# Kernel tuning notes

Measured on AMD Instinct MI355X. Metric: run time of the kernel, lower is better.

Reference implementation:

```python
import jax, jax.numpy as jnp
import numpy as np
import math

HIDDEN = 256
INPUT_SIZE = 32

def setup_inputs() -> dict:
    key = jax.random.key(0)
    k1, k2, k3 = jax.random.split(key, 3)
    stdv = 1.0 / math.sqrt(HIDDEN)
    inp = jax.random.normal(k1, (32, 48, 24, INPUT_SIZE), dtype=jnp.float32)
    W = jax.random.uniform(k2, (6 * HIDDEN, INPUT_SIZE + 2 * HIDDEN), minval=-stdv, maxval=stdv, dtype=jnp.float32)
    Bp = jax.random.uniform(k3, (6 * HIDDEN,), minval=-stdv, maxval=stdv, dtype=jnp.float32)
    return {"input": inp, "W": W, "Bp": Bp}

def _witran_forward(input, W, Bp):
    B, rows, cols, C = input.shape
    H = W.shape[0] // 6
    # flag == 1: permute to (cols, batch, rows, C)
    x = jnp.transpose(input, (2, 0, 1, 3))
    R = cols            # Water2sea_slice_num
    Lorig = rows        # Original_slice_len
    L = R + Lorig - 1   # Water2sea_slice_len
    # input_transfer: row r occupies slice positions r : r+Lorig (pad then roll)
    padded = jnp.pad(x, ((0, 0), (0, 0), (0, R - 1), (0, 0)))        # (R, B, L, C)
    shifted = jax.vmap(lambda xr, r: jnp.roll(xr, r, axis=1))(padded, jnp.arange(R))
    a = shifted.reshape(R * B, L, C)
    a_slices = jnp.transpose(a, (1, 0, 2))                            # (L, R*B, C)
    r_idx = jnp.repeat(jnp.arange(R), B)                              # (R*B,)

    def step(carry, inp):
        h_row, h_col = carry
        s, xs = inp
        # bias applied only to first (s+1)*B rows and only while s < R (faithful to torch)
        mask = ((r_idx <= s) & (s < R)).astype(xs.dtype)[:, None]
        gate = jnp.concatenate([h_row, h_col, xs], axis=-1) @ W.T + mask * Bp
        sig = jax.nn.sigmoid(gate[:, : 4 * H])
        tg = jnp.tanh(gate[:, 4 * H:])
        u_row, o_row, u_col, o_col = jnp.split(sig, 4, axis=-1)
        i_row, i_col = jnp.split(tg, 2, axis=-1)
        h_row = jnp.tanh((1.0 - u_row) * h_row + u_row * i_row) * o_row
        h_col_new = jnp.tanh((1.0 - u_col) * h_col + u_col * i_col) * o_col
        # roll col hidden down by one batch block for next diagonal
        h_col_rolled = jnp.roll(h_col_new, B, axis=0)
        return (h_row, h_col_rolled), (h_row, h_col_new)

    init = (jnp.zeros((R * B, H), input.dtype), jnp.zeros((R * B, H), input.dtype))
    _, (rows_all, cols_all) = jax.lax.scan(step, init, (jnp.arange(L), a_slices))
    # output_all_slice: stack along slice dim -> (R*B, L, 2H)
    output_all = jnp.transpose(jnp.concatenate([rows_all, cols_all], axis=-1), (1, 0, 2))
    rows_r = rows_all.reshape(L, R, B, H)
    cols_r = cols_all.reshape(L, R, B, H)
    # row hidden saved at slice s = Lorig-1+k from block k (diagonal)
    hidden_row = rows_r[jnp.arange(Lorig - 1, L), jnp.arange(R)]      # (R, B, H)
    # col hidden saved at slices s >= R-1 from the last block (pre-roll)
    hidden_col = cols_r[R - 1:, R - 1]                                # (Lorig, B, H)
    hidden_row_all = jnp.transpose(hidden_row, (1, 0, 2)).reshape(B, 1, R, H)
    hidden_col_all = jnp.transpose(hidden_col, (1, 0, 2)).reshape(B, 1, Lorig, H)
    # flag == 1 return order: (output, hidden_col_all, hidden_row_all)
    return output_all, hidden_col_all, hidden_row_all

def reference(input, W, Bp):
    return _witran_forward(input, W, Bp)
```

## Files before the change

kernel.cpp:

```cpp
#include <hip/hip_runtime.h>
#include <cstddef>


namespace {
constexpr int H_   = 256;
constexpr int R_   = 24;
constexpr int LOR_ = 48;
constexpr int L_   = 71;
constexpr int N_   = 768;
constexpr int KH_  = 512;
constexpr int KT_  = 544;
constexpr int AST_ = 552;
}

typedef __attribute__((ext_vector_type(8))) _Float16       f16x8;
typedef __attribute__((ext_vector_type(8))) unsigned short u16x8;
typedef __attribute__((ext_vector_type(4))) float          f32x4;
typedef __attribute__((ext_vector_type(2))) float          f32x2;

__device__ __forceinline__ float fsig(float x)  { return 1.f / (1.f + __expf(-x)); }
__device__ __forceinline__ float ftanhf(float x){ float e = __expf(2.f * x); return 1.f - 2.f / (e + 1.f); }

__global__ __launch_bounds__(256) void prep_all(const float* __restrict__ W,
                                                const float* __restrict__ inp,
                                                _Float16* __restrict__ Wfrag,
                                                _Float16* __restrict__ xall,
                                                unsigned long long* __restrict__ zb) {
    const int bx = blockIdx.x;
    const int t  = threadIdx.x;
    if (bx < 3264) {
        int o = bx * 256 + t;
        int j8   = o & 7;
        int lane = (o >> 3) & 63;
        int rest = o >> 9;
        int lt   = rest % 96;
        int kc   = rest / 96;
        int n0 = lane & 15, quad = lane >> 4;
        int lg  = lt * 16 + n0;
        int kt  = lg / 96;
        int rem = lg % 96;
        int g  = rem >> 4, kl = rem & 15;
        int j  = g * 256 + kt * 16 + kl;
        int kg = kc * 32 + quad * 8 + j8;
        Wfrag[o] = (_Float16)W[j * KT_ + kg];
    } else if (bx < 10080) {
        int o = (bx - 3264) * 256 + t;
        int c = o & 31;
        int n = (o >> 5) % N_;
        int s = (o >> 5) / N_;
        int r = n >> 5, b = n & 31;
        int l = s - r;
        float v = 0.f;
        if (l >= 0 && l < LOR_) v = inp[((b * LOR_ + l) * R_ + r) * 32 + c];
        xall[o] = (_Float16)v;
    } else {
        zb[(bx - 10080) * 256 + t] = 0ull;
    }
}

__global__ __launch_bounds__(384, 2) void step_k(
    const _Float16* __restrict__ Wfrag,
    const _Float16* __restrict__ xall,
    const _Float16* __restrict__ hbc,
    _Float16*       __restrict__ hbn,
    const float* __restrict__ Bp,
    float* __restrict__ out0, float* __restrict__ out1, float* __restrict__ out2,
    int s)
{
    __shared__ unsigned short As[48 * AST_];
    __shared__ float Gt[48][98];

    const int t    = threadIdx.x;
    const int wv   = t >> 6;
    const int lane = t & 63;
    const int n0   = lane & 15;
    const int quad = lane >> 4;
    const int kt   = blockIdx.x & 15;
    const int mc   = blockIdx.x >> 4;

    f16x8 bfr[17];
#pragma unroll
    for (int kc = 0; kc < 17; ++kc)
        bfr[kc] = *(const f16x8*)(const void*)(
            Wfrag + ((size_t)(kc * 96 + kt * 6 + wv) * 64 + lane) * 8);

    f16x8 xf[3];
#pragma unroll
    for (int mt = 0; mt < 3; ++mt)
        xf[mt] = *(const f16x8*)(const void*)(
            xall + ((size_t)(s * N_ + mc * 48 + mt * 16 + n0)) * 32 + quad * 8);

    const int mm = t >> 3;
    const int kp = (t & 7) * 2;
    const int n  = mc * 48 + mm;
    const int k  = kt * 16 + kp;
    f32x2 bp[6];
    if (s < R_) {
#pragma unroll
        for (int g = 0; g < 6; ++g)
            bp[g] = *(const f32x2*)(const void*)(Bp + g * 256 + k);
    }

#pragma unroll
    for (int it = 0; it < 8; ++it) {
        int q   = it * 384 + t;
        int row = q >> 6;
        int col = (q & 63) * 8;
        *(u16x8*)(void*)(&As[row * AST_ + col]) =
            *(const u16x8*)(const void*)((const unsigned short*)hbc +
                                         (size_t)(mc * 48 + row) * KH_ + col);
    }
    __syncthreads();

    f32x4 acc[3];
#pragma unroll
    for (int mt = 0; mt < 3; ++mt) acc[mt] = (f32x4){0.f, 0.f, 0.f, 0.f};

#pragma unroll
    for (int kc = 0; kc < 16; ++kc) {
        f16x8 a[3];
#pragma unroll
        for (int mt = 0; mt < 3; ++mt)
            a[mt] = *(const f16x8*)(const void*)(
                &As[(mt * 16 + n0) * AST_ + kc * 32 + quad * 8]);
#pragma unroll
        for (int mt = 0; mt < 3; ++mt)
            acc[mt] = __builtin_amdgcn_mfma_f32_16x16x32_f16(a[mt], bfr[kc], acc[mt], 0, 0, 0);
    }
#pragma unroll
    for (int mt = 0; mt < 3; ++mt)
        acc[mt] = __builtin_amdgcn_mfma_f32_16x16x32_f16(xf[mt], bfr[16], acc[mt], 0, 0, 0);

#pragma unroll
    for (int mt = 0; mt < 3; ++mt)
#pragma unroll
        for (int reg = 0; reg < 4; ++reg)
            Gt[mt * 16 + quad * 4 + reg][wv * 16 + n0] = acc[mt][reg];

    __syncthreads();

    {
        const int r  = n >> 5, b = n & 31;
        const bool useb = (r <= s) && (s < R_);

        f32x2 gv[6];
#pragma unroll
        for (int g = 0; g < 6; ++g) {
            f32x2 v = *(const f32x2*)(const void*)&Gt[mm][g * 16 + kp];
            gv[g] = useb ? (v + bp[g]) : v;
        }

        const _Float16* hrow = (const _Float16*)(const void*)&As[mm * AST_ + k];
        const _Float16* hcol = (const _Float16*)(const void*)&As[mm * AST_ + 256 + k];
        f32x2 hro = { (float)hrow[0], (float)hrow[1] };
        f32x2 hco = { (float)hcol[0], (float)hcol[1] };

        f32x2 hrv, hcv;
#pragma unroll
        for (int j = 0; j < 2; ++j) {
            float ur = fsig(gv[0][j]);
            float oR = fsig(gv[1][j]);
            float uc = fsig(gv[2][j]);
            float oc = fsig(gv[3][j]);
            float ir = ftanhf(gv[4][j]);
            float ic = ftanhf(gv[5][j]);
            hrv[j] = ftanhf((1.f - ur) * hro[j] + ur * ir) * oR;
            hcv[j] = ftanhf((1.f - uc) * hco[j] + uc * ic) * oc;
        }

        float* o0 = out0 + ((size_t)n * L_ + s) * 512;
        __builtin_nontemporal_store(hrv, (f32x2*)(void*)(o0 + k));
        __builtin_nontemporal_store(hcv, (f32x2*)(void*)(o0 + 256 + k));

        int n2 = n + 32; if (n2 >= N_) n2 -= N_;

        union { _Float16 h[2]; unsigned int u; } pr, pc;
        pr.h[0] = (_Float16)hrv[0]; pr.h[1] = (_Float16)hrv[1];
        pc.h[0] = (_Float16)hcv[0]; pc.h[1] = (_Float16)hcv[1];
        *(unsigned int*)(void*)(hbn + (size_t)n  * KH_ + k)       = pr.u;
        *(unsigned int*)(void*)(hbn + (size_t)n2 * KH_ + 256 + k) = pc.u;

        if (s >= LOR_ - 1 && r == s - (LOR_ - 1))
            __builtin_nontemporal_store(hrv, (f32x2*)(void*)(out2 + (size_t)(b * R_ + r) * H_ + k));
        if (r == R_ - 1 && s >= R_ - 1)
            __builtin_nontemporal_store(hcv, (f32x2*)(void*)(out1 + (size_t)(b * LOR_ + (s - (R_ - 1))) * H_ + k));
    }
}

extern "C" void kernel_launch(void* const* d_in, const int* in_sizes, int n_in,
                              void* d_out, int out_size, void* d_ws, size_t ws_size,
                              hipStream_t stream) {
    const float* inp = (const float*)d_in[0];
    const float* W   = (const float*)d_in[1];
    const float* Bp  = (const float*)d_in[2];

    float* out0 = (float*)d_out;
    float* out1 = out0 + (size_t)N_ * L_ * 512;
    float* out2 = out1 + (size_t)32 * LOR_ * H_;

    char* ws = (char*)d_ws;
    _Float16* Wfrag = (_Float16*)(ws);
    _Float16* xall  = (_Float16*)(ws + 1671168);
    _Float16* hb0   = (_Float16*)(ws + 5160960);
    _Float16* hb1   = (_Float16*)(ws + 5947392);

    prep_all<<<10848, 256, 0, stream>>>(W, inp, Wfrag, xall,
                                        (unsigned long long*)hb0);

    for (int s = 0; s < L_; ++s) {
        const _Float16* hbc = (s & 1) ? hb1 : hb0;
        _Float16*       hbn = (s & 1) ? hb0 : hb1;
        int act = (s < 23 ? s : 23) + 1;
        int nmc = (32 * act + 47) / 48;
        step_k<<<nmc * 16, 384, 0, stream>>>(Wfrag, xall, hbc, hbn,
                                             Bp, out0, out1, out2, s);
    }
}
```

Before: 616.6 us.

## Split K reduction across two wave groups with 768-thread blocks

Doubles the block to 768 threads and splits the 17 MFMA K-chunks between two groups of six waves. Each group writes partial gate sums to its own shared-memory tile, and the epilogue adds the two tiles before the gate activations. Each thread now handles one output element instead of two. For steps from 22 onward, the block-index mapping is also permuted to interleave mc across blocks. The aim is to halve per-wave serial MFMA latency and register pressure in this latency-bound per-step kernel, at the cost of more shared memory, an extra reduction, and narrower stores.

```diff
diff --git a/kernel.cpp b/kernel.cpp
--- a/kernel.cpp
+++ b/kernel.cpp
@@ -16,7 +16,6 @@
 typedef __attribute__((ext_vector_type(8))) _Float16       f16x8;
 typedef __attribute__((ext_vector_type(8))) unsigned short u16x8;
 typedef __attribute__((ext_vector_type(4))) float          f32x4;
-typedef __attribute__((ext_vector_type(2))) float          f32x2;
 
 __device__ __forceinline__ float fsig(float x)  { return 1.f / (1.f + __expf(-x)); }
 __device__ __forceinline__ float ftanhf(float x){ float e = __expf(2.f * x); return 1.f - 2.f / (e + 1.f); }
@@ -58,7 +57,7 @@
     }
 }
 
-__global__ __launch_bounds__(384, 2) void step_k(
+__global__ __launch_bounds__(768, 3) void step_k(
     const _Float16* __restrict__ Wfrag,
     const _Float16* __restrict__ xall,
     const _Float16* __restrict__ hbc,
@@ -68,42 +67,57 @@
     int s)
 {
     __shared__ unsigned short As[48 * AST_];
-    __shared__ float Gt[48][98];
+    __shared__ float Gt[2][48][98];
 
     const int t    = threadIdx.x;
     const int wv   = t >> 6;
     const int lane = t & 63;
     const int n0   = lane & 15;
     const int quad = lane >> 4;
-    const int kt   = blockIdx.x & 15;
-    const int mc   = blockIdx.x >> 4;
-
-    f16x8 bfr[17];
-#pragma unroll
-    for (int kc = 0; kc < 17; ++kc)
-        bfr[kc] = *(const f16x8*)(const void*)(
-            Wfrag + ((size_t)(kc * 96 + kt * 6 + wv) * 64 + lane) * 8);
-
+
+    int kt, mc;
+    if (s >= 22) {
+        int x = blockIdx.x & 7, q = blockIdx.x >> 3;
+        kt = q & 15; mc = ((q >> 4) << 3) | x;
+    } else {
+        kt = blockIdx.x & 15; mc = blockIdx.x >> 4;
+    }
+
+    const bool hi = (wv >= 6);
+    const int  g  = hi ? wv - 6 : wv;
+
+    f16x8 bfr[9];
     f16x8 xf[3];
-#pragma unroll
-    for (int mt = 0; mt < 3; ++mt)
-        xf[mt] = *(const f16x8*)(const void*)(
-            xall + ((size_t)(s * N_ + mc * 48 + mt * 16 + n0)) * 32 + quad * 8);
-
-    const int mm = t >> 3;
-    const int kp = (t & 7) * 2;
+    if (!hi) {
+#pragma unroll
+        for (int i = 0; i < 9; ++i)
+            bfr[i] = *(const f16x8*)(const void*)(
+                Wfrag + ((size_t)(i * 96 + kt * 6 + g) * 64 + lane) * 8);
+    } else {
+#pragma unroll
+        for (int i = 0; i < 8; ++i)
+            bfr[i] = *(const f16x8*)(const void*)(
+                Wfrag + ((size_t)((9 + i) * 96 + kt * 6 + g) * 64 + lane) * 8);
+#pragma unroll
+        for (int mt = 0; mt < 3; ++mt)
+            xf[mt] = *(const f16x8*)(const void*)(
+                xall + ((size_t)(s * N_ + mc * 48 + mt * 16 + n0)) * 32 + quad * 8);
+    }
+
+    const int mm = t >> 4;
+    const int kp = t & 15;
     const int n  = mc * 48 + mm;
     const int k  = kt * 16 + kp;
-    f32x2 bp[6];
+    float bp[6];
     if (s < R_) {
 #pragma unroll
-        for (int g = 0; g < 6; ++g)
-            bp[g] = *(const f32x2*)(const void*)(Bp + g * 256 + k);
-    }
-
-#pragma unroll
-    for (int it = 0; it < 8; ++it) {
-        int q   = it * 384 + t;
+        for (int gg = 0; gg < 6; ++gg)
+            bp[gg] = Bp[gg * 256 + k];
+    }
+
+#pragma unroll
+    for (int it = 0; it < 4; ++it) {
+        int q   = it * 768 + t;
         int row = q >> 6;
         int col = (q & 63) * 8;
         *(u16x8*)(void*)(&As[row * AST_ + col]) =
@@ -116,74 +130,77 @@
 #pragma unroll
     for (int mt = 0; mt < 3; ++mt) acc[mt] = (f32x4){0.f, 0.f, 0.f, 0.f};
 
-#pragma unroll
-    for (int kc = 0; kc < 16; ++kc) {
-        f16x8 a[3];
+    if (!hi) {
+#pragma unroll
+        for (int i = 0; i < 9; ++i) {
+            f16x8 a[3];
+#pragma unroll
+            for (int mt = 0; mt < 3; ++mt)
+                a[mt] = *(const f16x8*)(const void*)(
+                    &As[(mt * 16 + n0) * AST_ + i * 32 + quad * 8]);
+#pragma unroll
+            for (int mt = 0; mt < 3; ++mt)
+                acc[mt] = __builtin_amdgcn_mfma_f32_16x16x32_f16(a[mt], bfr[i], acc[mt], 0, 0, 0);
+        }
+    } else {
+#pragma unroll
+        for (int i = 0; i < 7; ++i) {
+            f16x8 a[3];
+#pragma unroll
+            for (int mt = 0; mt < 3; ++mt)
+                a[mt] = *(const f16x8*)(const void*)(
+                    &As[(mt * 16 + n0) * AST_ + (9 + i) * 32 + quad * 8]);
+#pragma unroll
+            for (int mt = 0; mt < 3; ++mt)
+                acc[mt] = __builtin_amdgcn_mfma_f32_16x16x32_f16(a[mt], bfr[i], acc[mt], 0, 0, 0);
+        }
 #pragma unroll
         for (int mt = 0; mt < 3; ++mt)
-            a[mt] = *(const f16x8*)(const void*)(
-                &As[(mt * 16 + n0) * AST_ + kc * 32 + quad * 8]);
+            acc[mt] = __builtin_amdgcn_mfma_f32_16x16x32_f16(xf[mt], bfr[7], acc[mt], 0, 0, 0);
+    }
+
+    {
+        float (*gt)[98] = Gt[hi ? 1 : 0];
 #pragma unroll
         for (int mt = 0; mt < 3; ++mt)
-            acc[mt] = __builtin_amdgcn_mfma_f32_16x16x32_f16(a[mt], bfr[kc], acc[mt], 0, 0, 0);
-    }
-#pragma unroll
-    for (int mt = 0; mt < 3; ++mt)
-        acc[mt] = __builtin_amdgcn_mfma_f32_16x16x32_f16(xf[mt], bfr[16], acc[mt], 0, 0, 0);
-
-#pragma unroll
-    for (int mt = 0; mt < 3; ++mt)
-#pragma unroll
-        for (int reg = 0; reg < 4; ++reg)
-            Gt[mt * 16 + quad * 4 + reg][wv * 16 + n0] = acc[mt][reg];
-
+#pragma unroll
+            for (int reg = 0; reg < 4; ++reg)
+                gt[mt * 16 + quad * 4 + reg][g * 16 + n0] = acc[mt][reg];
+    }
     __syncthreads();
 
     {
         const int r  = n >> 5, b = n & 31;
         const bool useb = (r <= s) && (s < R_);
 
-        f32x2 gv[6];
-#pragma unroll
-        for (int g = 0; g < 6; ++g) {
-            f32x2 v = *(const f32x2*)(const void*)&Gt[mm][g * 16 + kp];
-            gv[g] = useb ? (v + bp[g]) : v;
+        float gv[6];
+#pragma unroll
+        for (int gg = 0; gg < 6; ++gg) {
+            float v = Gt[0][mm][gg * 16 + kp] + Gt[1][mm][gg * 16 + kp];
+            gv[gg] = useb ? (v + bp[gg]) : v;
         }
 
-        const _Float16* hrow = (const _Float16*)(const void*)&As[mm * AST_ + k];
-        const _Float16* hcol = (const _Float16*)(const void*)&As[mm * AST_ + 256 + k];
-        f32x2 hro = { (float)hrow[0], (float)hrow[1] };
-        f32x2 hco = { (float)hcol[0], (float)hcol[1] };
-
-        f32x2 hrv, hcv;
-#pragma unroll
-        for (int j = 0; j < 2; ++j) {
-            float ur = fsig(gv[0][j]);
-            float oR = fsig(gv[1][j]);
-            float uc = fsig(gv[2][j]);
-            float oc = fsig(gv[3][j]);
-            float ir = ftanhf(gv[4][j]);
-            float ic = ftanhf(gv[5][j]);
-            hrv[j] = ftanhf((1.f - ur) * hro[j] + ur * ir) * oR;
-            hcv[j] = ftanhf((1.f - uc) * hco[j] + uc * ic) * oc;
-        }
+        float hro = (float)*(const _Float16*)(const void*)&As[mm * AST_ + k];
+        float hco = (float)*(const _Float16*)(const void*)&As[mm * AST_ + 256 + k];
+
+        float ur = fsig(gv[0]), oR = fsig(gv[1]);
+        float uc = fsig(gv[2]), oc = fsig(gv[3]);
+        float ir = ftanhf(gv[4]), ic = ftanhf(gv[5]);
+        float hrv = ftanhf((1.f - ur) * hro + ur * ir) * oR;
+        float hcv = ftanhf((1.f - uc) * hco + uc * ic) * oc;
 
         float* o0 = out0 + ((size_t)n * L_ + s) * 512;
-        __builtin_nontemporal_store(hrv, (f32x2*)(void*)(o0 + k));
-        __builtin_nontemporal_store(hcv, (f32x2*)(void*)(o0 + 256 + k));
+        __builtin_nontemporal_store(hrv, o0 + k);
+        __builtin_nontemporal_store(hcv, o0 + 256 + k);
 
         int n2 = n + 32; if (n2 >= N_) n2 -= N_;
-
-        union { _Float16 h[2]; unsigned int u; } pr, pc;
-        pr.h[0] = (_Float16)hrv[0]; pr.h[1] = (_Float16)hrv[1];
-        pc.h[0] = (_Float16)hcv[0]; pc.h[1] = (_Float16)hcv[1];
-        *(unsigned int*)(void*)(hbn + (size_t)n  * KH_ + k)       = pr.u;
-        *(unsigned int*)(void*)(hbn + (size_t)n2 * KH_ + 256 + k) = pc.u;
+        hbn[(size_t)n  * KH_ + k]       = (_Float16)hrv;
+        hbn[(size_t)n2 * KH_ + 256 + k] = (_Float16)hcv;
 
         if (s >= LOR_ - 1 && r == s - (LOR_ - 1))
-            __builtin_nontemporal_store(hrv, (f32x2*)(void*)(out2 + (size_t)(b * R_ + r) * H_ + k));
+            __builtin_nontemporal_store(hrv, out2 + (size_t)(b * R_ + r) * H_ + k);
         if (r == R_ - 1 && s >= R_ - 1)
-            __builtin_nontemporal_store(hcv, (f32x2*)(void*)(out1 + (size_t)(b * LOR_ + (s - (R_ - 1))) * H_ + k));
+            __builtin_nontemporal_store(hcv, out1 + (size_t)(b * LOR_ + (s - (R_ - 1))) * H_ + k);
     }
 }
 
@@ -212,7 +229,7 @@
         _Float16*       hbn = (s & 1) ? hb0 : hb1;
         int act = (s < 23 ? s : 23) + 1;
         int nmc = (32 * act + 47) / 48;
-        step_k<<<nmc * 16, 384, 0, stream>>>(Wfrag, xall, hbc, hbn,
+        step_k<<<nmc * 16, 768, 0, stream>>>(Wfrag, xall, hbc, hbn,
                                              Bp, out0, out1, out2, s);
     }
 }
```

New measurement: 579.1 us. -6.1%, faster.
